# Kernel optimization log

Hardware: AMD Instinct MI355X
Metric: run time of the kernel (lower is better)

## Reference

```python
import jax, jax.numpy as jnp
import numpy as np
from jax import lax

B, C, L, G = 2048, 9605, 20, 50
ALPHA, ALPHA1, ALPHA2, ALPHA3, ALPHA_OTHER = 0.5, 0.05, 2.0, 10.0, 0.5
NEG_INF = jnp.float32(-1e30)


def setup_inputs() -> dict:
    k0, k1, k2, k3 = jax.random.split(jax.random.key(0), 4)
    x = jax.random.normal(k0, (B, C), jnp.float32)
    # sparse multi-label targets (~10 positives/row) so at most ~1 whitelist group is active,
    # matching the original code's assert len(gt_whitelist_index) == 1
    y = (jax.random.uniform(k1, (B, C)) < 0.001).astype(jnp.int32)
    y_neg = (jax.random.uniform(k2, (B, C)) < 0.001).astype(jnp.int32)
    # L disjoint whitelist groups of G classes each (from mapping_dict in the original)
    idx = jax.random.permutation(k3, C)[: L * G].reshape(L, G)
    group_mask = jnp.zeros((L, C), bool).at[jnp.arange(L)[:, None], idx].set(True)
    return {"x": x, "y": y, "y_neg": y_neg, "group_mask": group_mask}


def _rank_loss(x1, x2, margin):
    # our_rank_loss: sigmoid(alpha3*(x2-x1+margin)), scaled by alpha2 when positive
    d = x2 - x1 + margin
    s = jax.nn.sigmoid(ALPHA3 * d)
    return jnp.where(d > 0, ALPHA2 * s, s)


def reference(x, y, y_neg, group_mask):
    xs = jax.nn.sigmoid(x)  # [B, C]
    gmf = group_mask.astype(jnp.float32)  # [L, C]

    # per-row max score inside each whitelist group -> [B, L]
    # lax.map over the L (=20) groups keeps peak memory at one [B, C] temp per step
    group_max = lax.map(
        lambda m: jnp.max(jnp.where(m, xs, NEG_INF), axis=-1), group_mask
    ).T  # [B, L]

    # find_gt_whitelist: group k active iff sum(y[group_k]) > 0
    active = jnp.einsum("bc,lc->bl", y.astype(jnp.float32), gmf) > 0
    active_neg = jnp.einsum("bc,lc->bl", y_neg.astype(jnp.float32), gmf) > 0
    has_gt = jnp.any(active, axis=-1)  # [B]
    g = jnp.argmax(active, axis=-1)  # first active group (original asserts exactly one)

    # top_k_thres = max(11th largest sigmoid score, alpha_other) in both branches
    thres = jnp.maximum(lax.top_k(xs, 11)[0][:, 10], ALPHA_OTHER)  # [B]

    # max over union of all whitelist classes (wl_indices)
    union_max = jnp.max(jnp.where(jnp.any(group_mask, 0)[None, :], xs, NEG_INF), -1)

    gt_max = jnp.take_along_axis(group_max, g[:, None], axis=1)[:, 0]  # [B]
    # incorrect_max: max(0, max over groups != g); incorrect_neg: max(0, max over neg-active groups)
    excl = jnp.where(jnp.arange(L)[None, :] == g[:, None], NEG_INF, group_max)
    incorrect_max = jnp.maximum(jnp.max(excl, -1), 0.0)
    incorrect_neg = jnp.maximum(jnp.max(jnp.where(active_neg, group_max, 0.0), -1), 0.0)

    # branch A: no gt whitelist group active
    case_a = (1 - ALPHA) * _rank_loss(thres, union_max, ALPHA1) + ALPHA * _rank_loss(
        thres, incorrect_neg, ALPHA1
    )
    # branch B: exactly one gt group g
    case_b = (
        _rank_loss(gt_max, thres, ALPHA1)
        + jnp.where(
            incorrect_max > 0, (1 - ALPHA) * _rank_loss(thres, incorrect_max, ALPHA1), 0.0
        )
        + jnp.where(
            incorrect_neg > 0,
            ALPHA * _rank_loss(thres, incorrect_neg, ALPHA1),
            ALPHA * _rank_loss(thres, incorrect_max, ALPHA1),
        )
    )
    return jnp.sum(jnp.where(has_gt, case_b, case_a))
```

## Files before the change

### kernel.cpp

```cpp
#include <hip/hip_runtime.h>
#include <stdint.h>

#define B_ROWS 2048
#define C_CLS  9605
#define L_GRP  20
#define GM_BYTES (L_GRP * C_CLS)
#define REPSTRIDE 9728
#define NEG_BIG -3.0e38f

__device__ __forceinline__ float sigmoidf(float v) {
  return 1.0f / (1.0f + __expf(-v));
}

__device__ __forceinline__ float rank_loss(float x1, float x2) {
  float d = x2 - x1 + 0.05f;
  float s = 1.0f / (1.0f + __expf(-10.0f * d));
  return d > 0.0f ? 2.0f * s : s;
}

__device__ __forceinline__ unsigned fmap(float f) {
  unsigned u = __float_as_uint(f);
  return (u & 0x80000000u) ? ~u : (u | 0x80000000u);
}
__device__ __forceinline__ float funmap(unsigned m) {
  unsigned u = (m & 0x80000000u) ? (m ^ 0x80000000u) : ~m;
  return __uint_as_float(u);
}

__global__ void probe_init_kernel(const uint4* __restrict__ gm,
                                  unsigned char* __restrict__ ws,
                                  float* __restrict__ out,
                                  int* __restrict__ flag) {
  __shared__ int s_part[16];
  const int tid = threadIdx.x;
  if (tid == 0) out[0] = 0.0f;
  const int initbytes = 3 * REPSTRIDE + C_CLS + 16;
  for (int i = tid; i < initbytes; i += 1024) ws[64 + i] = 0xFF;
  int local = 0;
  const int nvec = GM_BYTES / 16;
  for (int i = tid; i < nvec; i += 1024) {
    uint4 w = gm[i];
    unsigned a[4] = {w.x, w.y, w.z, w.w};
#pragma unroll
    for (int q = 0; q < 4; ++q) {
      local += ((a[q] & 0x000000FFu) != 0) + ((a[q] & 0x0000FF00u) != 0) +
               ((a[q] & 0x00FF0000u) != 0) + ((a[q] & 0xFF000000u) != 0);
    }
  }
  if (tid == 0) {
    const unsigned char* gb = (const unsigned char*)gm;
    for (int i = nvec * 16; i < GM_BYTES; ++i) local += (gb[i] != 0);
  }
#pragma unroll
  for (int off = 32; off; off >>= 1) local += __shfl_xor(local, off);
  if ((tid & 63) == 0) s_part[tid >> 6] = local;
  __syncthreads();
  if (tid == 0) {
    int tot = 0;
    for (int w = 0; w < 16; ++w) tot += s_part[w];
    *flag = tot;
  }
}

__global__ void build_gid_kernel(const void* gm, const int* __restrict__ flag,
                                 unsigned char* __restrict__ ws) {
  int i = blockIdx.x * blockDim.x + threadIdx.x;
  if (i >= GM_BYTES) return;
  const bool is_byte = (*flag > 600);
  bool m;
  if (is_byte) m = ((const unsigned char*)gm)[i] != 0;
  else         m = ((const unsigned int*)gm)[i] != 0u;
  if (m) {
    int l = i / C_CLS;
    int c = i - l * C_CLS;
    unsigned char* base = ws + 64;
#pragma unroll
    for (int r = 0; r < 4; ++r) base[r * REPSTRIDE + r + c] = (unsigned char)l;
  }
}

__global__ __launch_bounds__(256, 4) void loss_kernel(
    const float* __restrict__ x, const int* __restrict__ y,
    const int* __restrict__ yn, const unsigned char* __restrict__ ws64,
    float* __restrict__ out) {
  __shared__ unsigned s_gmax[L_GRP];
  __shared__ unsigned s_act, s_actn;
  __shared__ float s_wtop[4 * 11];
  const int tid = threadIdx.x;
  const int lane = tid & 63;
  const int wave = tid >> 6;
  const int row = blockIdx.x;

  const size_t base = (size_t)row * C_CLS;
  const int mis = (int)(base & 3);
  const int peel = (4 - mis) & 3;
  const float* xr = x + base;
  const int* yr = y + base;
  const int* nr = yn + base;
  const unsigned char* gidc = ws64 + mis * REPSTRIDE + mis;

  if (tid < L_GRP) s_gmax[tid] = 0u;
  if (tid == 0) { s_act = 0u; s_actn = 0u; }
  __syncthreads();

  float t[11];
#pragma unroll
  for (int i = 0; i < 11; ++i) t[i] = NEG_BIG;
  unsigned actL = 0u, actnL = 0u;

  auto process = [&](float v, unsigned gk, int yv, int nv) {
    if (v > t[10]) {
      float a = v;
#pragma unroll
      for (int i = 0; i < 11; ++i) {
        float hi = fmaxf(t[i], a); a = fminf(t[i], a); t[i] = hi;
      }
    }
    if (gk < L_GRP) {
      atomicMax(&s_gmax[gk], fmap(v));
      unsigned bit = 1u << gk;
      if (yv != 0) actL |= bit;
      if (nv != 0) actnL |= bit;
    }
  };

  if (tid < peel) process(xr[tid], gidc[tid], yr[tid], nr[tid]);

  const int nvec = (C_CLS - peel) >> 2;
  const float4* x4 = (const float4*)(xr + peel);
  const int4* y4 = (const int4*)(yr + peel);
  const int4* n4 = (const int4*)(nr + peel);
  const unsigned* g4 = (const unsigned*)(gidc + peel);
  for (int j = tid; j < nvec; j += 256) {
    float4 xv = x4[j];
    int4 yv = y4[j];
    int4 nv = n4[j];
    unsigned gw = g4[j];
    process(xv.x, gw & 0xFFu, yv.x, nv.x);
    process(xv.y, (gw >> 8) & 0xFFu, yv.y, nv.y);
    process(xv.z, (gw >> 16) & 0xFFu, yv.z, nv.z);
    process(xv.w, gw >> 24, yv.w, nv.w);
  }
  const int tail0 = peel + (nvec << 2);
  const int rem = C_CLS - tail0;
  if (tid < rem) {
    int c = tail0 + tid;
    process(xr[c], gidc[c], yr[c], nr[c]);
  }

  if (actL) atomicOr(&s_act, actL);
  if (actnL) atomicOr(&s_actn, actnL);

  float cur = t[0];
  float mr[11];
#pragma unroll
  for (int r = 0; r < 11; ++r) {
    float m = cur;
#pragma unroll
    for (int off = 32; off; off >>= 1) m = fmaxf(m, __shfl_xor(m, off));
    mr[r] = m;
    if (r < 10) {
      unsigned long long b = __ballot(cur == m);
      int leader = (int)(__ffsll(b) - 1);
      if (lane == leader) {
#pragma unroll
        for (int i = 0; i < 10; ++i) t[i] = t[i + 1];
        t[10] = NEG_BIG;
        cur = t[0];
      }
    }
  }
  if (lane == 0) {
#pragma unroll
    for (int r = 0; r < 11; ++r) s_wtop[wave * 11 + r] = mr[r];
  }
  __syncthreads();

  if (wave == 0) {
    float v = (lane < 44) ? s_wtop[lane] : NEG_BIG;
    float eleventh = NEG_BIG;
#pragma unroll
    for (int r = 0; r < 11; ++r) {
      float m = v;
#pragma unroll
      for (int off = 32; off; off >>= 1) m = fmaxf(m, __shfl_xor(m, off));
      eleventh = m;
      if (r < 10) {
        unsigned long long b = __ballot(v == m);
        int leader = (int)(__ffsll(b) - 1);
        if (lane == leader) v = NEG_BIG;
      }
    }

    const unsigned aL = s_act, anL = s_actn;
    const bool has_gt = (aL != 0u);
    const int g = has_gt ? (__ffs(aL) - 1) : 0;
    const float thres = fmaxf(sigmoidf(eleventh), 0.5f);

    float union_max = NEG_BIG, gt_sg = 0.0f, inc_max = NEG_BIG, inc_neg = 0.0f;
#pragma unroll
    for (int l = 0; l < L_GRP; ++l) {
      float sg = sigmoidf(funmap(s_gmax[l]));
      union_max = fmaxf(union_max, sg);
      if (l == g) gt_sg = sg; else inc_max = fmaxf(inc_max, sg);
      if ((anL >> l) & 1u) inc_neg = fmaxf(inc_neg, sg);
    }
    inc_max = fmaxf(inc_max, 0.0f);
    inc_neg = fmaxf(inc_neg, 0.0f);

    float loss;
    if (has_gt) {
      loss = rank_loss(gt_sg, thres);
      if (inc_max > 0.0f) loss += 0.5f * rank_loss(thres, inc_max);
      loss += 0.5f * rank_loss(thres, (inc_neg > 0.0f) ? inc_neg : inc_max);
    } else {
      loss = 0.5f * rank_loss(thres, union_max) + 0.5f * rank_loss(thres, inc_neg);
    }
    if (lane == 0) atomicAdd(out, loss);
  }
}

extern "C" void kernel_launch(void* const* d_in, const int* in_sizes, int n_in,
                              void* d_out, int out_size, void* d_ws, size_t ws_size,
                              hipStream_t stream) {
  (void)in_sizes; (void)n_in; (void)out_size; (void)ws_size;
  const float* x = (const float*)d_in[0];
  const int* y = (const int*)d_in[1];
  const int* yn = (const int*)d_in[2];
  const void* gm = d_in[3];

  int* flag = (int*)d_ws;
  unsigned char* ws = (unsigned char*)d_ws;
  unsigned char* ws64 = ws + 64;

  probe_init_kernel<<<1, 1024, 0, stream>>>((const uint4*)gm, ws,
                                            (float*)d_out, flag);
  build_gid_kernel<<<(GM_BYTES + 255) / 256, 256, 0, stream>>>(gm, flag, ws);
  loss_kernel<<<B_ROWS, 256, 0, stream>>>(x, y, yn, ws64, (float*)d_out);
}
```

Baseline: 252.8 us.

## Read y/y_neg only at whitelist positions via a compact class list

Builds a compact list of (class, group) entries for whitelist classes in the setup kernel and, in the loss kernel, reads y and y_neg only at those ~1000 positions instead of streaming the full int arrays. This removes roughly two thirds of the per-row global traffic. It also software-prefetches the next x/gid vector and skips the top-11 insertion when the max of four values is below the current threshold. The cost is an extra global atomic per whitelist entry during setup and scattered gathers of y/y_neg.

```diff
diff --git a/kernel.cpp b/kernel.cpp
--- a/kernel.cpp
+++ b/kernel.cpp
@@ -6,6 +6,8 @@
 #define L_GRP  20
 #define GM_BYTES (L_GRP * C_CLS)
 #define REPSTRIDE 9728
+#define LIST_OFF  39040
+#define LIST_CAP  16384
 #define NEG_BIG -3.0e38f
 
 __device__ __forceinline__ float sigmoidf(float v) {
@@ -27,15 +29,26 @@
   return __uint_as_float(u);
 }
 
+#define INS1(ti) { float hi = fmaxf(ti, a); a = fminf(ti, a); ti = hi; }
+#define INSERT(v)                                                         \
+  do {                                                                    \
+    if ((v) > t10) {                                                      \
+      float a = (v);                                                      \
+      INS1(t0) INS1(t1) INS1(t2) INS1(t3) INS1(t4) INS1(t5) INS1(t6)      \
+      INS1(t7) INS1(t8) INS1(t9) INS1(t10)                                \
+    }                                                                     \
+  } while (0)
+
 __global__ void probe_init_kernel(const uint4* __restrict__ gm,
                                   unsigned char* __restrict__ ws,
-                                  float* __restrict__ out,
-                                  int* __restrict__ flag) {
+                                  float* __restrict__ out) {
   __shared__ int s_part[16];
   const int tid = threadIdx.x;
-  if (tid == 0) out[0] = 0.0f;
-  const int initbytes = 3 * REPSTRIDE + C_CLS + 16;
-  for (int i = tid; i < initbytes; i += 1024) ws[64 + i] = 0xFF;
+  if (tid == 0) {
+    out[0] = 0.0f;
+    ((int*)ws)[1] = 0;
+  }
+  for (int i = tid; i < 4 * REPSTRIDE; i += 1024) ws[64 + i] = 0xFF;
   int local = 0;
   const int nvec = GM_BYTES / 16;
   for (int i = tid; i < nvec; i += 1024) {
@@ -58,15 +71,14 @@
   if (tid == 0) {
     int tot = 0;
     for (int w = 0; w < 16; ++w) tot += s_part[w];
-    *flag = tot;
-  }
-}
-
-__global__ void build_gid_kernel(const void* gm, const int* __restrict__ flag,
-                                 unsigned char* __restrict__ ws) {
+    ((int*)ws)[0] = tot;
+  }
+}
+
+__global__ void build_gid_kernel(const void* gm, unsigned char* __restrict__ ws) {
   int i = blockIdx.x * blockDim.x + threadIdx.x;
   if (i >= GM_BYTES) return;
-  const bool is_byte = (*flag > 600);
+  const bool is_byte = (((const int*)ws)[0] > 600);
   bool m;
   if (is_byte) m = ((const unsigned char*)gm)[i] != 0;
   else         m = ((const unsigned int*)gm)[i] != 0u;
@@ -76,12 +88,14 @@
     unsigned char* base = ws + 64;
 #pragma unroll
     for (int r = 0; r < 4; ++r) base[r * REPSTRIDE + r + c] = (unsigned char)l;
+    int slot = atomicAdd(&((int*)ws)[1], 1);
+    if (slot < LIST_CAP) ((int*)(ws + LIST_OFF))[slot] = c | (l << 16);
   }
 }
 
 __global__ __launch_bounds__(256, 4) void loss_kernel(
     const float* __restrict__ x, const int* __restrict__ y,
-    const int* __restrict__ yn, const unsigned char* __restrict__ ws64,
+    const int* __restrict__ yn, const unsigned char* __restrict__ ws,
     float* __restrict__ out) {
   __shared__ unsigned s_gmax[L_GRP];
   __shared__ unsigned s_act, s_actn;
@@ -97,61 +111,80 @@
   const float* xr = x + base;
   const int* yr = y + base;
   const int* nr = yn + base;
-  const unsigned char* gidc = ws64 + mis * REPSTRIDE + mis;
+  const unsigned char* gidc = ws + 64 + mis * REPSTRIDE + mis;
 
   if (tid < L_GRP) s_gmax[tid] = 0u;
   if (tid == 0) { s_act = 0u; s_actn = 0u; }
   __syncthreads();
 
-  float t[11];
-#pragma unroll
-  for (int i = 0; i < 11; ++i) t[i] = NEG_BIG;
-  unsigned actL = 0u, actnL = 0u;
-
-  auto process = [&](float v, unsigned gk, int yv, int nv) {
-    if (v > t[10]) {
-      float a = v;
-#pragma unroll
-      for (int i = 0; i < 11; ++i) {
-        float hi = fmaxf(t[i], a); a = fminf(t[i], a); t[i] = hi;
-      }
-    }
-    if (gk < L_GRP) {
-      atomicMax(&s_gmax[gk], fmap(v));
-      unsigned bit = 1u << gk;
-      if (yv != 0) actL |= bit;
-      if (nv != 0) actnL |= bit;
-    }
-  };
-
-  if (tid < peel) process(xr[tid], gidc[tid], yr[tid], nr[tid]);
+  float t0 = NEG_BIG, t1 = NEG_BIG, t2 = NEG_BIG, t3 = NEG_BIG, t4 = NEG_BIG,
+        t5 = NEG_BIG, t6 = NEG_BIG, t7 = NEG_BIG, t8 = NEG_BIG, t9 = NEG_BIG,
+        t10 = NEG_BIG;
+
+  if (tid < peel) {
+    float v = xr[tid];
+    INSERT(v);
+    unsigned gk = gidc[tid];
+    if (gk < L_GRP) atomicMax(&s_gmax[gk], fmap(v));
+  }
 
   const int nvec = (C_CLS - peel) >> 2;
   const float4* x4 = (const float4*)(xr + peel);
-  const int4* y4 = (const int4*)(yr + peel);
-  const int4* n4 = (const int4*)(nr + peel);
   const unsigned* g4 = (const unsigned*)(gidc + peel);
-  for (int j = tid; j < nvec; j += 256) {
-    float4 xv = x4[j];
-    int4 yv = y4[j];
-    int4 nv = n4[j];
-    unsigned gw = g4[j];
-    process(xv.x, gw & 0xFFu, yv.x, nv.x);
-    process(xv.y, (gw >> 8) & 0xFFu, yv.y, nv.y);
-    process(xv.z, (gw >> 16) & 0xFFu, yv.z, nv.z);
-    process(xv.w, gw >> 24, yv.w, nv.w);
-  }
+
+  int j = tid;
+  bool valid = j < nvec;
+  float4 xv = {0.f, 0.f, 0.f, 0.f};
+  unsigned gw = 0xFFFFFFFFu;
+  if (valid) { xv = x4[j]; gw = g4[j]; }
+  while (valid) {
+    const int jn = j + 256;
+    const bool vn = jn < nvec;
+    float4 xn = {0.f, 0.f, 0.f, 0.f};
+    unsigned gn = 0xFFFFFFFFu;
+    if (vn) { xn = x4[jn]; gn = g4[jn]; }
+
+    const float m4 = fmaxf(fmaxf(xv.x, xv.y), fmaxf(xv.z, xv.w));
+    if (m4 > t10) {
+      INSERT(xv.x); INSERT(xv.y); INSERT(xv.z); INSERT(xv.w);
+    }
+    if (gw != 0xFFFFFFFFu) {
+      const unsigned g0 = gw & 0xFFu, g1 = (gw >> 8) & 0xFFu;
+      const unsigned g2 = (gw >> 16) & 0xFFu, g3 = gw >> 24;
+      if (g0 < L_GRP) atomicMax(&s_gmax[g0], fmap(xv.x));
+      if (g1 < L_GRP) atomicMax(&s_gmax[g1], fmap(xv.y));
+      if (g2 < L_GRP) atomicMax(&s_gmax[g2], fmap(xv.z));
+      if (g3 < L_GRP) atomicMax(&s_gmax[g3], fmap(xv.w));
+    }
+    xv = xn; gw = gn; j = jn; valid = vn;
+  }
+
   const int tail0 = peel + (nvec << 2);
-  const int rem = C_CLS - tail0;
-  if (tid < rem) {
-    int c = tail0 + tid;
-    process(xr[c], gidc[c], yr[c], nr[c]);
-  }
-
-  if (actL) atomicOr(&s_act, actL);
-  if (actnL) atomicOr(&s_actn, actnL);
-
-  float cur = t[0];
+  if (tid < C_CLS - tail0) {
+    const int c = tail0 + tid;
+    float v = xr[c];
+    INSERT(v);
+    unsigned gk = gidc[c];
+    if (gk < L_GRP) atomicMax(&s_gmax[gk], fmap(v));
+  }
+
+  {
+    const int cnt = ((const int*)ws)[1];
+    const int* list = (const int*)(ws + LIST_OFF);
+    const int n = cnt < LIST_CAP ? cnt : LIST_CAP;
+    unsigned aL = 0u, anL = 0u;
+    for (int i = tid; i < n; i += 256) {
+      const int e = list[i];
+      const int c = e & 0xFFFF;
+      const unsigned bit = 1u << (e >> 16);
+      if (yr[c] != 0) aL |= bit;
+      if (nr[c] != 0) anL |= bit;
+    }
+    if (aL) atomicOr(&s_act, aL);
+    if (anL) atomicOr(&s_actn, anL);
+  }
+
+  float cur = t0;
   float mr[11];
 #pragma unroll
   for (int r = 0; r < 11; ++r) {
@@ -163,10 +196,9 @@
       unsigned long long b = __ballot(cur == m);
       int leader = (int)(__ffsll(b) - 1);
       if (lane == leader) {
-#pragma unroll
-        for (int i = 0; i < 10; ++i) t[i] = t[i + 1];
-        t[10] = NEG_BIG;
-        cur = t[0];
+        t0 = t1; t1 = t2; t2 = t3; t3 = t4; t4 = t5; t5 = t6; t6 = t7;
+        t7 = t8; t8 = t9; t9 = t10; t10 = NEG_BIG;
+        cur = t0;
       }
     }
   }
@@ -229,12 +261,9 @@
   const int* yn = (const int*)d_in[2];
   const void* gm = d_in[3];
 
-  int* flag = (int*)d_ws;
   unsigned char* ws = (unsigned char*)d_ws;
-  unsigned char* ws64 = ws + 64;
-
-  probe_init_kernel<<<1, 1024, 0, stream>>>((const uint4*)gm, ws,
-                                            (float*)d_out, flag);
-  build_gid_kernel<<<(GM_BYTES + 255) / 256, 256, 0, stream>>>(gm, flag, ws);
-  loss_kernel<<<B_ROWS, 256, 0, stream>>>(x, y, yn, ws64, (float*)d_out);
-}
+
+  probe_init_kernel<<<1, 1024, 0, stream>>>((const uint4*)gm, ws, (float*)d_out);
+  build_gid_kernel<<<(GM_BYTES + 255) / 256, 256, 0, stream>>>(gm, ws);
+  loss_kernel<<<B_ROWS, 256, 0, stream>>>(x, y, yn, ws, (float*)d_out);
+}
```

After: 262.3 us. 1.04x slower.
